# Performance work log

Hardware: AMD Instinct MI355X
Metric: run time of the kernel (lower is better)

Reference implementation:

```python
import jax, jax.numpy as jnp
import numpy as np

B, S, D, VOCAB, K = 32, 128, 300, 20000, 8


def setup_inputs() -> dict:
    key = jax.random.key(0)
    ks = jax.random.split(key, 12)
    return {
        "words": jax.random.normal(ks[0], (B, S, D), jnp.float32),
        "lengths": jax.random.randint(ks[1], (B,), S // 2, S + 1),
        "vocab": jax.random.normal(ks[2], (VOCAB, D), jnp.float32) * 0.1,
        "default_embed": jax.random.uniform(ks[3], (D,), jnp.float32),
        "W": jnp.eye(D, dtype=jnp.float32) + 0.01 * jax.random.normal(ks[4], (D, D), jnp.float32),
        "lstm_Wih": jax.random.normal(ks[5], (4 * D, D), jnp.float32) * 0.05,
        "lstm_Whh": jax.random.normal(ks[6], (4 * D, D), jnp.float32) * 0.05,
        "lstm_bih": jnp.zeros((4 * D,), jnp.float32),
        "lstm_bhh": jnp.zeros((4 * D,), jnp.float32),
        "rnn_Wih": jax.random.normal(ks[7], (D, D), jnp.float32) * 0.05,
        "rnn_Whh": jax.random.normal(ks[8], (D, D), jnp.float32) * 0.05,
        "rnn_bih": jnp.zeros((D,), jnp.float32),
        "rnn_bhh": jnp.zeros((D,), jnp.float32),
    }


def _forward(words, lengths, vocab, default_embed, W,
             lstm_Wih, lstm_Whh, lstm_bih, lstm_bhh,
             rnn_Wih, rnn_Whh, rnn_bih, rnn_bhh):
    b, s, d = words.shape
    # --- NormalizeWordsModel (tagger) ---
    C = jnp.concatenate([vocab.T, default_embed[:, None]], axis=1)  # [D, V+1]
    P = jax.nn.softmax(jnp.einsum("bsd,de,ev->bsv", words, W, C), axis=-1)  # [B,S,V+1]
    V = P[..., -1:] * words + jnp.einsum("bsv,vd->bsd", P[..., :-1], vocab)  # [B,S,D]

    # --- LSTM encoder, final hidden at true length (packed-sequence semantics) ---
    valid = (jnp.arange(s)[None, :] < lengths[:, None])  # [B,S]

    def lstm_step(carry, xs):
        h, c = carry
        x_t, v_t = xs  # [B,D], [B]
        gates = x_t @ lstm_Wih.T + lstm_bih + h @ lstm_Whh.T + lstm_bhh  # [B,4D]
        i, f, g, o = jnp.split(gates, 4, axis=-1)
        c_new = jax.nn.sigmoid(f) * c + jax.nn.sigmoid(i) * jnp.tanh(g)
        h_new = jax.nn.sigmoid(o) * jnp.tanh(c_new)
        m = v_t[:, None]
        h = jnp.where(m, h_new, h)
        c = jnp.where(m, c_new, c)
        return (h, c), None

    h0 = jnp.zeros((b, d), V.dtype)
    (q, _), _ = jax.lax.scan(lstm_step, (h0, h0),
                             (jnp.swapaxes(V, 0, 1), valid.T))  # q: [B,D]

    # --- InstructionsDecoder: RNNCell applied K times to the same input q ---
    def rnn_step(h, _):
        h2 = jnp.tanh(q @ rnn_Wih.T + rnn_bih + h @ rnn_Whh.T + rnn_bhh)
        return h2, h2

    _, H = jax.lax.scan(rnn_step, h0, None, length=K)  # [K,B,D]
    H = jnp.swapaxes(H, 0, 1)  # [B,K,D]

    # --- masked softmax attention readout ---
    scores = jnp.einsum("bkd,bsd->bks", H, V)  # [B,K,S]
    scores = jnp.where(valid[:, None, :], scores, -jnp.inf)
    R = jnp.einsum("bks,bsd->bkd", jax.nn.softmax(scores, axis=-1), V)
    return R


def reference(words, lengths, vocab, default_embed, W,
              lstm_Wih, lstm_Whh, lstm_bih, lstm_bhh,
              rnn_Wih, rnn_Whh, rnn_bih, rnn_bhh):
    return _forward(words, lengths, vocab, default_embed, W,
                    lstm_Wih, lstm_Whh, lstm_bih, lstm_bhh,
                    rnn_Wih, rnn_Whh, rnn_bih, rnn_bhh)
```

## Files before the change

### kernel.cpp

```cpp
#include <hip/hip_runtime.h>


typedef unsigned short u16;
typedef unsigned int   u32;
typedef float  f32x4 __attribute__((ext_vector_type(4)));
typedef u32    u32x4 __attribute__((ext_vector_type(4)));
typedef __bf16 bf16x8 __attribute__((ext_vector_type(8)));
typedef _Float16 f16x2 __attribute__((ext_vector_type(2)));
typedef _Float16 f16x8 __attribute__((ext_vector_type(8)));

#define SCOPE_AGENT __HIP_MEMORY_SCOPE_AGENT

__device__ __forceinline__ float bf2f(u16 u) { return __uint_as_float(((u32)u) << 16); }
__device__ __forceinline__ u16 f2bf(float f) {
  u32 x = __float_as_uint(f);
  u32 r = (x + 0x7fffu + ((x >> 16) & 1u)) >> 16;
  return (u16)r;
}
__device__ __forceinline__ float sigm(float x) { return 1.f / (1.f + __expf(-x)); }
__device__ __forceinline__ u16 f2h(float f) {
  union { _Float16 h; u16 u; } cv; cv.h = (_Float16)f; return cv.u;
}
__device__ __forceinline__ float h2f(u16 u) {
  union { _Float16 h; u16 u; } cv; cv.u = u; return (float)cv.h;
}

template <int CTRL>
__device__ __forceinline__ float dppmv(float v) {
  return __uint_as_float(
      (u32)__builtin_amdgcn_mov_dpp((int)__float_as_uint(v), CTRL, 0xF, 0xF, true));
}

__device__ __forceinline__ void stage_chunk(const u16* __restrict__ pA,
                                            const u16* __restrict__ pB,
                                            int ci, u16* dst, int tid) {
  const u32x4* gA = (const u32x4*)pA + (size_t)ci * 1280;
  const u32x4* gB = (const u32x4*)pB + (size_t)ci * 1216;
  u32x4* sb = (u32x4*)dst;
#pragma unroll
  for (int i = 0; i < 5; i++) {
    int idx = tid + i * 512;
    if (idx < 2496) {
      const u32x4* g = (idx < 1280) ? (gA + idx) : (gB + (idx - 1280));
      __builtin_amdgcn_global_load_lds(
          (const __attribute__((address_space(1))) u32*)(const u32*)g,
          (__attribute__((address_space(3))) u32*)(u32*)(sb + idx), 16, 0, 0);
    }
  }
}

__device__ __forceinline__ void conv_seg(const void* src, u16* dst, int n, int is32,
                                         int t0, int stride) {
  if (is32) {
    const float* s = (const float*)src;
    for (int i = t0; i < n; i += stride) dst[i] = f2bf(s[i]);
  } else {
    const u16* s = (const u16*)src;
    for (int i = t0; i < n; i += stride) dst[i] = s[i];
  }
}

__global__ __launch_bounds__(256) void k_ingest(
    const void* words, const void* vocab, const void* de, const void* W,
    const void* lWih, const void* lWhh, const void* lbih, const void* lbhh,
    const void* rWih, const void* rWhh, const void* rbih, const void* rbhh,
    u16* cw, u16* cv, u16* cde, u16* cW, u16* cWih, u16* cWhh, u16* cbih, u16* cbhh,
    u16* crWih, u16* crWhh, u16* crbih, u16* crbhh, u32* flag, u32* seqz, u32* hbz) {
  __shared__ int s_is32;
  int tid = threadIdx.x;
  int vote = 0;
  if (tid < 64) {
    u32 w = ((const u32*)words)[tid];
    int e = (w >> 7) & 0xFF;
    vote = (e >= 100 && e <= 150) ? 1 : 0;
  }
  unsigned long long m = __ballot(vote);
  if (tid == 0) s_is32 = (__popcll(m) < 32) ? 1 : 0;
  __syncthreads();
  int is32 = s_is32;
  if (blockIdx.x == 0 && tid == 0) *flag = (u32)is32;
  int t0 = blockIdx.x * 256 + tid;
  int stride = gridDim.x * 256;
  if (t0 < 256) seqz[t0] = 0;
  if (t0 < 10240) hbz[t0] = 0;
  conv_seg(words, cw, 1228800, is32, t0, stride);
  conv_seg(vocab, cv, 6000000, is32, t0, stride);
  conv_seg(de, cde, 300, is32, t0, stride);
  conv_seg(W, cW, 90000, is32, t0, stride);
  conv_seg(lWih, cWih, 360000, is32, t0, stride);
  conv_seg(lWhh, cWhh, 360000, is32, t0, stride);
  conv_seg(lbih, cbih, 1200, is32, t0, stride);
  conv_seg(lbhh, cbhh, 1200, is32, t0, stride);
  conv_seg(rWih, crWih, 90000, is32, t0, stride);
  conv_seg(rWhh, crWhh, 90000, is32, t0, stride);
  conv_seg(rbih, crbih, 300, is32, t0, stride);
  conv_seg(rbhh, crbhh, 300, is32, t0, stride);
}

__global__ __launch_bounds__(256) void k_transpose_bf(const u16* __restrict__ in,
                                                      u16* __restrict__ out,
                                                      int J, int K) {
  __shared__ u16 t[32][33];
  int j0 = blockIdx.x * 32, k0 = blockIdx.y * 32;
  int lx = threadIdx.x & 31, ly = threadIdx.x >> 5;
  for (int r = ly; r < 32; r += 8) {
    int j = j0 + r, k = k0 + lx;
    t[r][lx] = (j < J && k < K) ? in[(size_t)j * K + k] : (u16)0;
  }
  __syncthreads();
  for (int r = ly; r < 32; r += 8) {
    int k = k0 + r, j = j0 + lx;
    if (k < K && j < J) out[(size_t)k * J + j] = t[lx][r];
  }
}

__global__ __launch_bounds__(256) void k_pack_w8(const u16* __restrict__ Whh,
                                                 u16* __restrict__ pW) {
  int idx = blockIdx.x * 256 + threadIdx.x;
  if (idx >= 409600) return;
  int bid = idx / 51200;
  int r = idx - bid * 51200;
  int j = r & 7;
  int lane = (r >> 3) & 63;
  int t2 = r >> 9;
  int kt = t2 % 10, w = t2 / 10;
  int n16 = lane & 15, quad = lane >> 4;
  int n = w * 16 + n16;
  int gate = n / 40, dl = n - gate * 40;
  int nd = (bid < 7) ? 38 : 34;
  int dim = 38 * bid + dl;
  int k = kt * 32 + quad * 8 + j;
  u16 out = 0;
  if (dl < nd && k < 300)
    out = f2h(bf2f(Whh[(size_t)(gate * 300 + dim) * 300 + k]));
  pW[idx] = out;
}

__global__ __launch_bounds__(256) void k_pack_vocab(const u16* __restrict__ vocab,
                                                    u16* __restrict__ pA,
                                                    u16* __restrict__ pB) {
  __shared__ u16 sv[32][320];
  int ci = blockIdx.x, tid = threadIdx.x;
  for (int idx = tid; idx < 32 * 20; idx += 256) {
    int v = idx / 20, k = 300 + (idx - v * 20);
    sv[v][k] = 0;
  }
  for (int idx = tid; idx < 32 * 300; idx += 256) {
    int v = idx / 300, k = idx - v * 300;
    sv[v][k] = vocab[(size_t)(ci * 32 + v) * 300 + k];
  }
  __syncthreads();
  for (int idx = tid; idx < 10240; idx += 256) {
    int j = idx & 7, lane = (idx >> 3) & 63, t2 = idx >> 9;
    int kk = t2 % 10, h = t2 / 10;
    int v = h * 16 + (lane & 15);
    int k = kk * 32 + ((lane >> 4)) * 8 + j;
    pA[(size_t)ci * 10240 + (size_t)idx] = sv[v][k];
  }
  for (int idx = tid; idx < 9728; idx += 256) {
    int j = idx & 7, lane = (idx >> 3) & 63, nc = idx >> 9;
    int v = (lane >> 4) * 8 + j;
    int n = nc * 16 + (lane & 15);
    pB[(size_t)ci * 9728 + (size_t)idx] = sv[v][n];
  }
}

__global__ __launch_bounds__(256) void k_xw(const u16* __restrict__ words,
                                            const u16* __restrict__ W,
                                            u16* __restrict__ X) {
  __shared__ float As[300][33];
  int n0 = blockIdx.x * 128;
  int r0 = blockIdx.y * 32;
  int tid = threadIdx.x;
  for (int idx = tid; idx < 32 * 300; idx += 256) {
    int r = idx / 300, k = idx - r * 300;
    As[k][r] = bf2f(words[(size_t)(r0 + r) * 300 + k]);
  }
  __syncthreads();
  int j = n0 + (tid & 127);
  int rh = (tid >> 7) * 16;
  float acc[16];
#pragma unroll
  for (int i = 0; i < 16; i++) acc[i] = 0.f;
  if (j < 300) {
    for (int k = 0; k < 300; k++) {
      float bw = bf2f(W[(size_t)k * 300 + j]);
#pragma unroll
      for (int i = 0; i < 16; i++) acc[i] += As[k][rh + i] * bw;
    }
  }
  if (j < 320) {
#pragma unroll
    for (int i = 0; i < 16; i++) {
      float v = (j < 300) ? acc[i] : 0.f;
      X[(size_t)(r0 + rh + i) * 320 + j] = f2bf(v);
    }
  }
}

__global__ __launch_bounds__(512, 2) void k_softmax_v(
    const u16* __restrict__ X, const u16* __restrict__ pA, const u16* __restrict__ pB,
    u16* __restrict__ pAcc, float* __restrict__ pML) {
  __shared__ __align__(16) u16 chunk[2][19968];
  __shared__ __align__(16) float ptbuf[8 * 576];
  int bid = blockIdx.x;
  int sl = bid & 7, b = bid >> 3;
  int tid = threadIdx.x;
  int w = tid >> 6, lane = tid & 63;
  int quad = lane >> 4, n16 = lane & 15;
  int cs = (sl == 0) ? 0 : 79 + (sl - 1) * 78;
  int nch = (sl == 0) ? 79 : 78;

  int rowA = b * 128 + w * 16 + n16;
  const bf16x8* Xrow = (const bf16x8*)(X + (size_t)rowA * 320);
  bf16x8 afr[10];
#pragma unroll
  for (int kk = 0; kk < 10; kk++) afr[kk] = Xrow[kk * 4 + quad];

  f32x4 acc[19];
#pragma unroll
  for (int i = 0; i < 19; i++) { acc[i][0] = 0.f; acc[i][1] = 0.f; acc[i][2] = 0.f; acc[i][3] = 0.f; }
  f32x4 mrun, lrun;
#pragma unroll
  for (int c = 0; c < 4; c++) { mrun[c] = -1e30f; lrun[c] = 0.f; }
  float* myPt = ptbuf + w * 576;

  stage_chunk(pA, pB, cs, &chunk[0][0], tid);
  __syncthreads();

  int cur = 0;
  for (int ic = 0; ic < nch; ic++) {
    if (ic + 1 < nch) stage_chunk(pA, pB, cs + ic + 1, &chunk[cur ^ 1][0], tid);
    const bf16x8* bufA = (const bf16x8*)&chunk[cur][0];
    const bf16x8* bufB = (const bf16x8*)&chunk[cur][10240];
    f32x4 L0, L1;
#pragma unroll
    for (int c = 0; c < 4; c++) { L0[c] = 0.f; L1[c] = 0.f; }
#pragma unroll
    for (int kk = 0; kk < 10; kk++) {
      L0 = __builtin_amdgcn_mfma_f32_16x16x32_bf16(afr[kk], bufA[kk * 64 + lane], L0, 0, 0, 0);
      L1 = __builtin_amdgcn_mfma_f32_16x16x32_bf16(afr[kk], bufA[(10 + kk) * 64 + lane], L1, 0, 0, 0);
    }
    f32x4 t;
#pragma unroll
    for (int c = 0; c < 4; c++) {
      float x = fmaxf(L0[c], L1[c]);
      x = fmaxf(x, dppmv<0xB1>(x));
      x = fmaxf(x, dppmv<0x4E>(x));
      x = fmaxf(x, dppmv<0x141>(x));
      x = fmaxf(x, dppmv<0x140>(x));
      t[c] = x;
    }
    f32x4 mnew, al, P0v, P1v, rs;
#pragma unroll
    for (int c = 0; c < 4; c++) {
      mnew[c] = fmaxf(mrun[c], t[c]);
      al[c] = __expf(mrun[c] - mnew[c]);
      P0v[c] = __expf(L0[c] - mnew[c]);
      P1v[c] = __expf(L1[c] - mnew[c]);
      rs[c] = P0v[c] + P1v[c];
    }
#pragma unroll
    for (int c = 0; c < 4; c++) {
      float x = rs[c];
      x += dppmv<0xB1>(x);
      x += dppmv<0x4E>(x);
      x += dppmv<0x141>(x);
      x += dppmv<0x140>(x);
      rs[c] = x;
    }
#pragma unroll
    for (int c = 0; c < 4; c++) { lrun[c] = lrun[c] * al[c] + rs[c]; mrun[c] = mnew[c]; }
#pragma unroll
    for (int r = 0; r < 4; r++) {
      myPt[(quad * 4 + r) * 36 + n16] = P0v[r];
      myPt[(quad * 4 + r) * 36 + 16 + n16] = P1v[r];
    }
    f32x4 plo = *(const f32x4*)(myPt + n16 * 36 + quad * 8);
    f32x4 phi = *(const f32x4*)(myPt + n16 * 36 + quad * 8 + 4);
    bf16x8 paf;
#pragma unroll
    for (int c = 0; c < 4; c++) { paf[c] = (__bf16)plo[c]; paf[c + 4] = (__bf16)phi[c]; }
#pragma unroll
    for (int nc = 0; nc < 19; nc++) {
      f32x4 a = acc[nc];
#pragma unroll
      for (int c = 0; c < 4; c++) a[c] *= al[c];
      acc[nc] = __builtin_amdgcn_mfma_f32_16x16x32_bf16(paf, bufB[nc * 64 + lane], a, 0, 0, 0);
    }
    __syncthreads();
    cur ^= 1;
  }

  size_t prow = (size_t)sl * 4096 + (size_t)b * 128 + w * 16;
  if (n16 == 0) {
#pragma unroll
    for (int r = 0; r < 4; r++) {
      pML[(prow + quad * 4 + r) * 2 + 0] = mrun[r];
      pML[(prow + quad * 4 + r) * 2 + 1] = lrun[r];
    }
  }
#pragma unroll
  for (int nc = 0; nc < 19; nc++)
#pragma unroll
    for (int r = 0; r < 4; r++)
      pAcc[(prow + quad * 4 + r) * 304 + nc * 16 + n16] = f2bf(acc[nc][r]);
}

__global__ __launch_bounds__(320) void k_combine(
    const u16* __restrict__ pAcc, const float* __restrict__ pML,
    const u16* __restrict__ X, const u16* __restrict__ de,
    const u16* __restrict__ words, u16* __restrict__ Vout) {
  __shared__ float red[320];
  __shared__ float fs[8];
  __shared__ float sinv, sw;
  int row = blockIdx.x, tid = threadIdx.x;
  float p = 0.f;
  if (tid < 300) p = bf2f(X[(size_t)row * 320 + tid]) * bf2f(de[tid]);
  red[tid] = p;
  __syncthreads();
  if (tid == 0) {
    float d = 0.f;
    for (int i = 0; i < 300; i++) d += red[i];
    float mv[8], lv[8], ms = -1e30f;
    for (int s = 0; s < 8; s++) {
      mv[s] = pML[((size_t)s * 4096 + row) * 2];
      lv[s] = pML[((size_t)s * 4096 + row) * 2 + 1];
      ms = fmaxf(ms, mv[s]);
    }
    float mf = fmaxf(ms, d);
    float pd = __expf(d - mf);
    float l = pd;
    for (int s = 0; s < 8; s++) {
      float f = __expf(mv[s] - mf);
      fs[s] = f;
      l += lv[s] * f;
    }
    sinv = 1.f / l;
    sw = pd / l;
  }
  __syncthreads();
  float v = 0.f;
  if (tid < 300) {
    float a = 0.f;
#pragma unroll
    for (int s = 0; s < 8; s++)
      a += bf2f(pAcc[((size_t)s * 4096 + row) * 304 + tid]) * fs[s];
    v = a * sinv + sw * bf2f(words[(size_t)row * 300 + tid]);
  }
  Vout[(size_t)row * 320 + tid] = f2bf(v);
}

__global__ __launch_bounds__(256) void k_xg(const u16* __restrict__ Vb,
                                            const u16* __restrict__ WihT,
                                            const u16* __restrict__ bih,
                                            const u16* __restrict__ bhh,
                                            float* __restrict__ xg) {
  __shared__ float As[300][33];
  int n0 = blockIdx.x * 128;
  int r0 = blockIdx.y * 32;
  int tid = threadIdx.x;
  for (int idx = tid; idx < 32 * 300; idx += 256) {
    int r = idx / 300, k = idx - r * 300;
    As[k][r] = bf2f(Vb[(size_t)(r0 + r) * 320 + k]);
  }
  __syncthreads();
  int j = n0 + (tid & 127);
  if (j >= 1200) return;
  int rh = (tid >> 7) * 16;
  float acc[16];
#pragma unroll
  for (int i = 0; i < 16; i++) acc[i] = 0.f;
  for (int k = 0; k < 300; k++) {
    float bw = bf2f(WihT[(size_t)k * 1200 + j]);
#pragma unroll
    for (int i = 0; i < 16; i++) acc[i] += As[k][rh + i] * bw;
  }
  float bias = bf2f(bih[j]) + bf2f(bhh[j]);
#pragma unroll
  for (int i = 0; i < 16; i++)
    xg[(size_t)(r0 + rh + i) * 1200 + j] = acc[i] + bias;
}

__global__ __launch_bounds__(640, 1) void k_lstm7(
    const float* __restrict__ xg, const u16* __restrict__ pW,
    const int* __restrict__ lengths, u16* __restrict__ hb, u32* __restrict__ seq) {
  __shared__ float gl[16][164];
  __shared__ int s_maxlen;
  int bidx = blockIdx.x;
  int mg = bidx >> 3, bid = bidx & 7;
  int tid = threadIdx.x;
  int w = tid >> 6, lane = tid & 63;
  int quad = lane >> 4, n16 = lane & 15;
  int nd = (bid < 7) ? 38 : 34;
  {
    int lv = (tid < 16) ? lengths[mg * 16 + tid] : 0;
    for (int off2 = 1; off2 < 16; off2 <<= 1) {
      int o = __shfl_xor(lv, off2, 64);
      lv = lv > o ? lv : o;
    }
    if (tid == 0) s_maxlen = lv;
  }
  f16x8 bf[10];
  const u32x4* pw4 = (const u32x4*)(pW + (size_t)bid * 51200);
#pragma unroll
  for (int kt = 0; kt < 10; kt++)
    bf[kt] = __builtin_bit_cast(f16x8, pw4[(w * 10 + kt) * 64 + lane]);
  int b0 = tid / 40, dl = tid - b0 * 40;
  bool a0 = dl < nd;
  int bg = mg * 16 + b0;
  int len0 = lengths[bg];
  int dim = 38 * bid + dl;
  int sa = (((dim >> 5)) * 64 + ((dim >> 3) & 3) * 16 + b0) * 8 + (dim & 7);
  float c0 = 0.f, h0 = 0.f;
  u32* myf = seq + (size_t)bidx * 16;
  __syncthreads();
  int maxlen = s_maxlen;
  for (int t = 0; t < maxlen; t++) {
    if (tid < 8) {
      while (__hip_atomic_load(&seq[(mg * 8 + tid) * 16], __ATOMIC_ACQUIRE, SCOPE_AGENT) < (u32)t)
        __builtin_amdgcn_s_sleep(2);
    }
    __syncthreads();
    float xv0 = 0.f, xv1 = 0.f, xv2 = 0.f, xv3 = 0.f;
    const float* xr0 = xg + ((size_t)bg * 128 + t) * 1200 + dim;
    if (a0) { xv0 = xr0[0]; xv1 = xr0[300]; xv2 = xr0[600]; xv3 = xr0[900]; }
    const u32x4* hbt = (const u32x4*)hb + (size_t)(mg * 2 + (t & 1)) * 640;
    u32x4 af[10];
#pragma unroll
    for (int kt = 0; kt < 10; kt++)
      af[kt] = hbt[kt * 64 + lane];
    f32x4 C;
    C[0] = 0.f; C[1] = 0.f; C[2] = 0.f; C[3] = 0.f;
#pragma unroll
    for (int kt = 0; kt < 10; kt++)
      C = __builtin_amdgcn_mfma_f32_16x16x32_f16(
          __builtin_bit_cast(f16x8, af[kt]), bf[kt], C, 0, 0, 0);
#pragma unroll
    for (int rr = 0; rr < 4; rr++)
      gl[quad * 4 + rr][w * 16 + n16] = C[rr];
    __syncthreads();
    u16* hbw = hb + (size_t)(mg * 2 + ((t + 1) & 1)) * 5120;
    if (a0) {
      float gi = gl[b0][dl] + xv0, gf = gl[b0][40 + dl] + xv1;
      float gg = gl[b0][80 + dl] + xv2, go = gl[b0][120 + dl] + xv3;
      if (t < len0) {
        c0 = sigm(gf) * c0 + sigm(gi) * tanhf(gg);
        h0 = sigm(go) * tanhf(c0);
      }
      hbw[sa] = f2h(h0);
    }
    __syncthreads();
    if (tid == 0)
      __hip_atomic_store(myf, (u32)(t + 1), __ATOMIC_RELEASE, SCOPE_AGENT);
  }
}

__global__ __launch_bounds__(320) void k_rnn(
    const u16* __restrict__ hb, const int* __restrict__ lengths,
    const u16* __restrict__ rWihT, const u16* __restrict__ rWhhT,
    const u16* __restrict__ rbih, const u16* __restrict__ rbhh,
    float* __restrict__ H) {
  __shared__ float qs[304], h2[304], base[304];
  __shared__ int s_maxlen;
  int b = blockIdx.x, tid = threadIdx.x;
  int mg = b >> 4;
  {
    int lv = (tid < 16) ? lengths[mg * 16 + tid] : 0;
    for (int off2 = 1; off2 < 16; off2 <<= 1) {
      int o = __shfl_xor(lv, off2, 64);
      lv = lv > o ? lv : o;
    }
    if (tid == 0) s_maxlen = lv;
  }
  __syncthreads();
  int buf = s_maxlen & 1;
  if (tid < 304) {
    float q = 0.f;
    if (tid < 300) {
      int dim = tid;
      int idx = ((dim >> 5) * 64 + ((dim >> 3) & 3) * 16 + (b & 15)) * 8 + (dim & 7);
      q = h2f(hb[(size_t)(mg * 2 + buf) * 5120 + idx]);
    }
    qs[tid] = q;
    h2[tid] = 0.f;
  }
  __syncthreads();
  if (tid < 300) {
    float a = bf2f(rbih[tid]) + bf2f(rbhh[tid]);
    for (int k = 0; k < 300; k++) a += qs[k] * bf2f(rWihT[(size_t)k * 300 + tid]);
    base[tid] = a;
  }
  __syncthreads();
  for (int s = 0; s < 8; s++) {
    float nv = 0.f;
    if (tid < 300) {
      float a = base[tid];
      for (int k = 0; k < 300; k++) a += h2[k] * bf2f(rWhhT[(size_t)k * 300 + tid]);
      nv = tanhf(a);
    }
    __syncthreads();
    if (tid < 300) {
      h2[tid] = nv;
      H[((size_t)b * 8 + s) * 300 + tid] = nv;
    }
    __syncthreads();
  }
}

__global__ __launch_bounds__(256) void k_attn(const float* __restrict__ H,
                                              const u16* __restrict__ Vb,
                                              const int* __restrict__ lengths,
                                              const u32* __restrict__ flag,
                                              void* __restrict__ dout) {
  __shared__ float Hs[8][304];
  __shared__ float sc[8][128];
  __shared__ float wsum[8];
  int b = blockIdx.x, tid = threadIdx.x;
  int len = lengths[b];
  int is32 = (int)*flag;
  for (int idx = tid; idx < 8 * 300; idx += 256) {
    int k = idx / 300, j = idx - k * 300;
    Hs[k][j] = H[((size_t)b * 8 + k) * 300 + j];
  }
  __syncthreads();
  for (int s = tid; s < len; s += 256) {
    const u16* vr = Vb + (size_t)(b * 128 + s) * 320;
    float a[8];
#pragma unroll
    for (int k = 0; k < 8; k++) a[k] = 0.f;
    for (int j = 0; j < 300; j++) {
      float v = bf2f(vr[j]);
#pragma unroll
      for (int k = 0; k < 8; k++) a[k] += Hs[k][j] * v;
    }
#pragma unroll
    for (int k = 0; k < 8; k++) sc[k][s] = a[k];
  }
  __syncthreads();
  if (tid < 8) {
    float m = -1e30f;
    for (int s = 0; s < len; s++) m = fmaxf(m, sc[tid][s]);
    float l = 0.f;
    for (int s = 0; s < len; s++) { float e = __expf(sc[tid][s] - m); sc[tid][s] = e; l += e; }
    wsum[tid] = 1.f / l;
  }
  __syncthreads();
  int k = tid >> 5, jl = tid & 31;
  for (int j = jl; j < 300; j += 32) {
    float a = 0.f;
    for (int s = 0; s < len; s++) a += sc[k][s] * bf2f(Vb[(size_t)(b * 128 + s) * 320 + j]);
    float val = a * wsum[k];
    size_t o = ((size_t)b * 8 + k) * 300 + j;
    if (is32) ((float*)dout)[o] = val;
    else ((u16*)dout)[o] = f2bf(val);
  }
}

extern "C" void kernel_launch(void* const* d_in, const int* in_sizes, int n_in,
                              void* d_out, int out_size, void* d_ws, size_t ws_size,
                              hipStream_t stream) {
  (void)in_sizes; (void)n_in; (void)out_size; (void)ws_size;
  const void* words = d_in[0];
  const int* lengths = (const int*)d_in[1];
  const void* vocab = d_in[2];
  const void* de = d_in[3];
  const void* W = d_in[4];
  const void* lWih = d_in[5];
  const void* lWhh = d_in[6];
  const void* lbih = d_in[7];
  const void* lbhh = d_in[8];
  const void* rWih = d_in[9];
  const void* rWhh = d_in[10];
  const void* rbih = d_in[11];
  const void* rbhh = d_in[12];

  char* basep = (char*)d_ws;
  size_t off = 0;
  auto take = [&](size_t bytes) -> char* {
    char* p = basep + off;
    off += (bytes + 255) & ~(size_t)255;
    return p;
  };
  u16* cw    = (u16*)take(1228800 * 2);
  u16* cv    = (u16*)take(6000000 * 2);
  u16* cde   = (u16*)take(300 * 2);
  u16* cW    = (u16*)take(90000 * 2);
  u16* cWih  = (u16*)take(360000 * 2);
  u16* cWhh  = (u16*)take(360000 * 2);
  u16* cbih  = (u16*)take(1200 * 2);
  u16* cbhh  = (u16*)take(1200 * 2);
  u16* crWih = (u16*)take(90000 * 2);
  u16* crWhh = (u16*)take(90000 * 2);
  u16* crbih = (u16*)take(300 * 2);
  u16* crbhh = (u16*)take(300 * 2);
  u32* flag  = (u32*)take(256);
  u16*   X     = (u16*)take((size_t)4096 * 320 * 2);
  u16*   Vb    = (u16*)take((size_t)4096 * 320 * 2);
  u16*   WihT  = (u16*)take((size_t)300 * 1200 * 2);
  u16*   pW8   = (u16*)take((size_t)409600 * 2);
  u16*   rWihT = (u16*)take((size_t)300 * 300 * 2);
  u16*   rWhhT = (u16*)take((size_t)300 * 300 * 2);
  u16*   pAcc  = (u16*)take((size_t)8 * 4096 * 304 * 2);
  float* pML   = (float*)take((size_t)8 * 4096 * 2 * 4);
  float* H     = (float*)take((size_t)32 * 8 * 300 * 4);
  u16*   hb    = (u16*)take((size_t)2 * 2 * 5120 * 2);
  u32*   seq   = (u32*)take((size_t)4096 * 4);
  char* ureg = take((size_t)25000192);
  u16*   pA = (u16*)ureg;
  u16*   pB = (u16*)(ureg + (size_t)625 * 10240 * 2);
  float* xg = (float*)ureg;

  k_ingest<<<4096, 256, 0, stream>>>(words, vocab, de, W, lWih, lWhh, lbih, lbhh,
                                     rWih, rWhh, rbih, rbhh,
                                     cw, cv, cde, cW, cWih, cWhh, cbih, cbhh,
                                     crWih, crWhh, crbih, crbhh, flag, seq, (u32*)hb);
  k_transpose_bf<<<dim3(38, 10), 256, 0, stream>>>(cWih, WihT, 1200, 300);
  k_transpose_bf<<<dim3(10, 10), 256, 0, stream>>>(crWih, rWihT, 300, 300);
  k_transpose_bf<<<dim3(10, 10), 256, 0, stream>>>(crWhh, rWhhT, 300, 300);
  k_pack_w8<<<1600, 256, 0, stream>>>(cWhh, pW8);
  k_pack_vocab<<<625, 256, 0, stream>>>(cv, pA, pB);
  k_xw<<<dim3(3, 128), 256, 0, stream>>>(cw, cW, X);
  k_softmax_v<<<256, 512, 0, stream>>>(X, pA, pB, pAcc, pML);
  k_combine<<<4096, 320, 0, stream>>>(pAcc, pML, X, cde, cw, Vb);
  k_xg<<<dim3(10, 128), 256, 0, stream>>>(Vb, WihT, cbih, cbhh, xg);
  k_lstm7<<<16, 640, 0, stream>>>(xg, pW8, lengths, hb, seq);
  k_rnn<<<32, 320, 0, stream>>>(hb, lengths, rWihT, rWhhT, crbih, crbhh, H);
  k_attn<<<32, 256, 0, stream>>>(H, Vb, lengths, flag, d_out);
}
```

Measured before the change: 990.6 us.

## Use MFMA for LSTM input projection and split attention per head

Packs the LSTM input weight into an MFMA-friendly fragment layout and rewrites the input-gate GEMM with bf16 16x16x32 MFMA instead of scalar FMAs over shared memory. The attention readout is split into one block per (batch, head) with wave-level shuffle reductions for max and sum, replacing serial single-thread loops. The combine kernel also replaces a serial 300-element sum with a shuffle reduction. A new packing kernel is added, and the attention split rereads V once per head.

```diff
diff --git a/kernel.cpp b/kernel.cpp
--- a/kernel.cpp
+++ b/kernel.cpp
@@ -136,6 +136,19 @@
   pW[idx] = out;
 }
 
+__global__ __launch_bounds__(256) void k_pack_wih(const u16* __restrict__ cWih,
+                                                  u16* __restrict__ pW) {
+  int idx = blockIdx.x * 256 + threadIdx.x;
+  if (idx >= 384000) return;
+  int j = idx & 7;
+  int lane = (idx >> 3) & 63;
+  int t2 = idx >> 9;
+  int kt = t2 % 10, nc = t2 / 10;
+  int n = nc * 16 + (lane & 15);
+  int k = kt * 32 + (lane >> 4) * 8 + j;
+  pW[idx] = (k < 300) ? cWih[(size_t)n * 300 + k] : (u16)0;
+}
+
 __global__ __launch_bounds__(256) void k_pack_vocab(const u16* __restrict__ vocab,
                                                     u16* __restrict__ pA,
                                                     u16* __restrict__ pB) {
@@ -319,9 +332,14 @@
   if (tid < 300) p = bf2f(X[(size_t)row * 320 + tid]) * bf2f(de[tid]);
   red[tid] = p;
   __syncthreads();
+  if (tid < 64) {
+    float s = red[tid] + red[tid + 64] + red[tid + 128] + red[tid + 192] + red[tid + 256];
+    for (int off = 32; off; off >>= 1) s += __shfl_xor(s, off, 64);
+    if (tid == 0) red[0] = s;
+  }
+  __syncthreads();
   if (tid == 0) {
-    float d = 0.f;
-    for (int i = 0; i < 300; i++) d += red[i];
+    float d = red[0];
     float mv[8], lv[8], ms = -1e30f;
     for (int s = 0; s < 8; s++) {
       mv[s] = pML[((size_t)s * 4096 + row) * 2];
@@ -352,34 +370,36 @@
 }
 
 __global__ __launch_bounds__(256) void k_xg(const u16* __restrict__ Vb,
-                                            const u16* __restrict__ WihT,
+                                            const u16* __restrict__ pWih,
                                             const u16* __restrict__ bih,
                                             const u16* __restrict__ bhh,
                                             float* __restrict__ xg) {
-  __shared__ float As[300][33];
-  int n0 = blockIdx.x * 128;
-  int r0 = blockIdx.y * 32;
+  int cb = blockIdx.x;
+  int rb = blockIdx.y;
   int tid = threadIdx.x;
-  for (int idx = tid; idx < 32 * 300; idx += 256) {
-    int r = idx / 300, k = idx - r * 300;
-    As[k][r] = bf2f(Vb[(size_t)(r0 + r) * 320 + k]);
-  }
-  __syncthreads();
-  int j = n0 + (tid & 127);
-  if (j >= 1200) return;
-  int rh = (tid >> 7) * 16;
-  float acc[16];
-#pragma unroll
-  for (int i = 0; i < 16; i++) acc[i] = 0.f;
-  for (int k = 0; k < 300; k++) {
-    float bw = bf2f(WihT[(size_t)k * 1200 + j]);
-#pragma unroll
-    for (int i = 0; i < 16; i++) acc[i] += As[k][rh + i] * bw;
-  }
-  float bias = bf2f(bih[j]) + bf2f(bhh[j]);
-#pragma unroll
-  for (int i = 0; i < 16; i++)
-    xg[(size_t)(r0 + rh + i) * 1200 + j] = acc[i] + bias;
+  int w = tid >> 6, lane = tid & 63;
+  int quad = lane >> 4, n16 = lane & 15;
+  int rowA = rb * 64 + w * 16 + n16;
+  const bf16x8* Xrow = (const bf16x8*)(Vb + (size_t)rowA * 320);
+  bf16x8 afr[10];
+#pragma unroll
+  for (int kt = 0; kt < 10; kt++) afr[kt] = Xrow[kt * 4 + quad];
+  const u32x4* pw4 = (const u32x4*)pWih;
+  int rb4 = rb * 64 + w * 16 + quad * 4;
+  for (int nc2 = 0; nc2 < 15; nc2++) {
+    int nc = cb * 15 + nc2;
+    f32x4 C;
+    C[0] = 0.f; C[1] = 0.f; C[2] = 0.f; C[3] = 0.f;
+#pragma unroll
+    for (int kt = 0; kt < 10; kt++)
+      C = __builtin_amdgcn_mfma_f32_16x16x32_bf16(
+          afr[kt], __builtin_bit_cast(bf16x8, pw4[(nc * 10 + kt) * 64 + lane]), C, 0, 0, 0);
+    int n = nc * 16 + n16;
+    float bias = bf2f(bih[n]) + bf2f(bhh[n]);
+#pragma unroll
+    for (int r = 0; r < 4; r++)
+      xg[(size_t)(rb4 + r) * 1200 + n] = C[r] + bias;
+  }
 }
 
 __global__ __launch_bounds__(640, 1) void k_lstm7(
@@ -513,44 +533,41 @@
                                               const int* __restrict__ lengths,
                                               const u32* __restrict__ flag,
                                               void* __restrict__ dout) {
-  __shared__ float Hs[8][304];
-  __shared__ float sc[8][128];
-  __shared__ float wsum[8];
-  int b = blockIdx.x, tid = threadIdx.x;
+  __shared__ float Hs[304];
+  __shared__ float sc[128];
+  __shared__ float winv;
+  int bid = blockIdx.x;
+  int b = bid >> 3, k = bid & 7;
+  int tid = threadIdx.x;
   int len = lengths[b];
   int is32 = (int)*flag;
-  for (int idx = tid; idx < 8 * 300; idx += 256) {
-    int k = idx / 300, j = idx - k * 300;
-    Hs[k][j] = H[((size_t)b * 8 + k) * 300 + j];
-  }
+  for (int j = tid; j < 300; j += 256) Hs[j] = H[((size_t)b * 8 + k) * 300 + j];
   __syncthreads();
   for (int s = tid; s < len; s += 256) {
     const u16* vr = Vb + (size_t)(b * 128 + s) * 320;
-    float a[8];
-#pragma unroll
-    for (int k = 0; k < 8; k++) a[k] = 0.f;
-    for (int j = 0; j < 300; j++) {
-      float v = bf2f(vr[j]);
-#pragma unroll
-      for (int k = 0; k < 8; k++) a[k] += Hs[k][j] * v;
-    }
-#pragma unroll
-    for (int k = 0; k < 8; k++) sc[k][s] = a[k];
-  }
-  __syncthreads();
-  if (tid < 8) {
-    float m = -1e30f;
-    for (int s = 0; s < len; s++) m = fmaxf(m, sc[tid][s]);
-    float l = 0.f;
-    for (int s = 0; s < len; s++) { float e = __expf(sc[tid][s] - m); sc[tid][s] = e; l += e; }
-    wsum[tid] = 1.f / l;
-  }
-  __syncthreads();
-  int k = tid >> 5, jl = tid & 31;
-  for (int j = jl; j < 300; j += 32) {
     float a = 0.f;
-    for (int s = 0; s < len; s++) a += sc[k][s] * bf2f(Vb[(size_t)(b * 128 + s) * 320 + j]);
-    float val = a * wsum[k];
+    for (int j = 0; j < 300; j++) a += Hs[j] * bf2f(vr[j]);
+    sc[s] = a;
+  }
+  __syncthreads();
+  if (tid < 64) {
+    float m = sc[tid];
+    if (tid + 64 < len) m = fmaxf(m, sc[tid + 64]);
+    for (int off = 32; off; off >>= 1) m = fmaxf(m, __shfl_xor(m, off, 64));
+    float e0 = __expf(sc[tid] - m);
+    sc[tid] = e0;
+    float e1 = 0.f;
+    if (tid + 64 < len) { e1 = __expf(sc[tid + 64] - m); sc[tid + 64] = e1; }
+    float l = e0 + e1;
+    for (int off = 32; off; off >>= 1) l += __shfl_xor(l, off, 64);
+    if (tid == 0) winv = 1.f / l;
+  }
+  __syncthreads();
+  float ws = winv;
+  for (int j = tid; j < 300; j += 256) {
+    float a = 0.f;
+    for (int s = 0; s < len; s++) a += sc[s] * bf2f(Vb[(size_t)(b * 128 + s) * 320 + j]);
+    float val = a * ws;
     size_t o = ((size_t)b * 8 + k) * 300 + j;
     if (is32) ((float*)dout)[o] = val;
     else ((u16*)dout)[o] = f2bf(val);
@@ -597,7 +614,7 @@
   u32* flag  = (u32*)take(256);
   u16*   X     = (u16*)take((size_t)4096 * 320 * 2);
   u16*   Vb    = (u16*)take((size_t)4096 * 320 * 2);
-  u16*   WihT  = (u16*)take((size_t)300 * 1200 * 2);
+  u16*   pWih  = (u16*)take((size_t)384000 * 2);
   u16*   pW8   = (u16*)take((size_t)409600 * 2);
   u16*   rWihT = (u16*)take((size_t)300 * 300 * 2);
   u16*   rWhhT = (u16*)take((size_t)300 * 300 * 2);
@@ -615,7 +632,7 @@
                                      rWih, rWhh, rbih, rbhh,
                                      cw, cv, cde, cW, cWih, cWhh, cbih, cbhh,
                                      crWih, crWhh, crbih, crbhh, flag, seq, (u32*)hb);
-  k_transpose_bf<<<dim3(38, 10), 256, 0, stream>>>(cWih, WihT, 1200, 300);
+  k_pack_wih<<<1500, 256, 0, stream>>>(cWih, pWih);
   k_transpose_bf<<<dim3(10, 10), 256, 0, stream>>>(crWih, rWihT, 300, 300);
   k_transpose_bf<<<dim3(10, 10), 256, 0, stream>>>(crWhh, rWhhT, 300, 300);
   k_pack_w8<<<1600, 256, 0, stream>>>(cWhh, pW8);
@@ -623,8 +640,8 @@
   k_xw<<<dim3(3, 128), 256, 0, stream>>>(cw, cW, X);
   k_softmax_v<<<256, 512, 0, stream>>>(X, pA, pB, pAcc, pML);
   k_combine<<<4096, 320, 0, stream>>>(pAcc, pML, X, cde, cw, Vb);
-  k_xg<<<dim3(10, 128), 256, 0, stream>>>(Vb, WihT, cbih, cbhh, xg);
+  k_xg<<<dim3(5, 64), 256, 0, stream>>>(Vb, pWih, cbih, cbhh, xg);
   k_lstm7<<<16, 640, 0, stream>>>(xg, pW8, lengths, hb, seq);
   k_rnn<<<32, 320, 0, stream>>>(hb, lengths, rWihT, rWhhT, crbih, crbhh, H);
-  k_attn<<<32, 256, 0, stream>>>(H, Vb, lengths, flag, d_out);
-}
+  k_attn<<<256, 256, 0, stream>>>(H, Vb, lengths, flag, d_out);
+}
```

Result: faster. 877.7 us (-11.4%).
